# Optimization experiments

Measured on AMD Instinct MI355X. Metric: run time of the kernel, lower is better.

The kernel has to match this reference:

```python
import jax, jax.numpy as jnp
import numpy as np

W_LOAD = 0.01  # config.w_load
CAP_FACTOR = 2  # expert capacity = CAP_FACTOR * tokens * top_k / n_experts


def setup_inputs() -> dict:
    key = jax.random.key(0)
    ks = jax.random.split(key, 8)
    B, T, d, E, dff = 4, 4096, 1024, 8, 4096
    N = B * T
    s = 0.02
    return {
        "x": jax.random.normal(ks[0], (B, T, d), jnp.float32),
        "noise": jax.random.normal(ks[1], (N, E), jnp.float32),
        "gate_w": jax.random.normal(ks[2], (d, E), jnp.float32) * s,
        "noise_w": jax.random.normal(ks[3], (d, E), jnp.float32) * s,
        "w1": jax.random.normal(ks[4], (E, d, dff), jnp.float32) * s,
        "b1": jnp.zeros((E, dff), jnp.float32),
        "w2": jax.random.normal(ks[5], (E, dff, d), jnp.float32) * s,
        "b2": jnp.zeros((E, d), jnp.float32),
        "top_k": 2,
    }


def _moe_forward(x, noise, gate_w, noise_w, w1, b1, w2, b2, top_k):
    B, T, d = x.shape
    N = B * T
    E = gate_w.shape[1]
    xs = x.reshape(N, d)

    # noisy gating
    gate_logits = xs @ gate_w                       # [N, E]
    noise_std = jax.nn.softplus(xs @ noise_w)       # [N, E]
    gate_logits = gate_logits + noise * noise_std

    # load loss: kth-largest logit excluding each expert i
    eye = jnp.eye(E, dtype=bool)
    masked = jnp.where(eye[None, :, :], -jnp.inf, gate_logits[:, None, :])  # [N,E,E]
    kth_excl = jax.lax.top_k(masked, top_k)[0][..., -1]                     # [N,E]
    P = jax.scipy.stats.norm.cdf((gate_logits - kth_excl) / noise_std)
    load = P.sum(axis=0)                            # [E]
    cv = jnp.std(load, ddof=1) / jnp.mean(load)     # torch .std() is unbiased
    load_loss = W_LOAD * cv ** 2

    # top-k routing weights (softmax over selected logits, in fp32)
    topk_vals, sel = jax.lax.top_k(gate_logits, top_k)          # [N,K]
    wts = jax.nn.softmax(topk_vals.astype(jnp.float32), axis=-1).astype(x.dtype)

    # dispatch: flatten (token, slot) pairs, compute position within each expert
    ef = sel.reshape(-1)                            # [N*K] expert id per pair
    tf = jnp.repeat(jnp.arange(N), top_k)           # [N*K] token id per pair
    wf = wts.reshape(-1)                            # [N*K] combine weight
    oh = jax.nn.one_hot(ef, E, dtype=jnp.int32)     # [N*K, E]
    pos = ((jnp.cumsum(oh, axis=0) - oh) * oh).sum(-1)  # slot index within expert

    C = (CAP_FACTOR * N * top_k) // E               # expert capacity (no drops in practice)
    buf = jnp.zeros((E, C, d), x.dtype).at[ef, pos].set(xs[tf], mode="drop")

    # grouped FFN per expert
    h = jax.nn.gelu(jnp.einsum("ecd,edh->ech", buf, w1) + b1[:, None, :], approximate=True)
    y = jnp.einsum("ech,ehd->ecd", h, w2) + b2[:, None, :]

    # combine: gather pair outputs, weight, scatter-add back to tokens
    valid = pos < C
    pair_out = y[ef, jnp.minimum(pos, C - 1)]       # [N*K, d]
    contrib = jnp.where(valid[:, None], wf[:, None] * pair_out, 0.0)
    results = jnp.zeros((N, d), x.dtype).at[tf].add(contrib)
    return results.reshape(B, T, d), load_loss


def reference(x, noise, gate_w, noise_w, w1, b1, w2, b2, top_k):
    return _moe_forward(x, noise, gate_w, noise_w, w1, b1, w2, b2, top_k)
```

## Files before the change

### kernel.cpp

```cpp
#include <hip/hip_runtime.h>
#include <stdint.h>

#define N_TOK   16384
#define DMODEL  1024
#define NEXP    8
#define DFF     4096
#define CAP     8192
#define MAXB    136
#define W_LOAD_C 0.01f

typedef __attribute__((ext_vector_type(8))) short short8;
typedef __attribute__((ext_vector_type(4))) float f32x4;

__device__ __forceinline__ uint16_t f2bf(float f) {
    uint32_t u = __float_as_uint(f);
    uint32_t r = u + 0x7fffu + ((u >> 16) & 1u);
    return (uint16_t)(r >> 16);
}
__device__ __forceinline__ float bf2f(uint16_t u) {
    return __uint_as_float((uint32_t)u << 16);
}

__device__ __forceinline__ float gelu_tanh(float v) {
    float u = 0.7978845608028654f * (v + 0.044715f * v * v * v);
    float ex = __expf(2.0f * u);
    float th = 1.0f - 2.0f / (ex + 1.0f);
    return 0.5f * v * (1.0f + th);
}

__device__ __forceinline__ void glds16(const uint16_t* g, uint16_t* l) {
    __builtin_amdgcn_global_load_lds(
        (const __attribute__((address_space(1))) void*)g,
        (__attribute__((address_space(3))) void*)l, 16, 0, 0);
}

__global__ __launch_bounds__(512) void gating_kernel(
    const float* __restrict__ x, const float* __restrict__ noise,
    const float* __restrict__ gate_w, const float* __restrict__ noise_w,
    int* __restrict__ cnt, float* __restrict__ loadAcc,
    int* __restrict__ rowlist, float* __restrict__ slotw,
    int* __restrict__ tpos0, int* __restrict__ tpos1,
    float* __restrict__ tw0, float* __restrict__ tw1,
    uint16_t* __restrict__ xb)
{
    __shared__ float lp[8][8];
    __shared__ int   se1[8], se2[8];
    __shared__ float sw1[8], sw2[8];

    const int lane = threadIdx.x & 63;
    const int wid  = threadIdx.x >> 6;
    const int t = blockIdx.x * 8 + wid;

    const float* xr = x + (size_t)t * DMODEL;
    uint16_t* xbr = xb + (size_t)t * DMODEL;
    float ag[8] = {0,0,0,0,0,0,0,0};
    float an[8] = {0,0,0,0,0,0,0,0};
    for (int j = 0; j < 16; ++j) {
        int idx = j * 64 + lane;
        float xv = xr[idx];
        xbr[idx] = f2bf(xv);
        const float4* gp  = (const float4*)(gate_w  + idx * 8);
        const float4* np_ = (const float4*)(noise_w + idx * 8);
        float4 g0 = gp[0], g1 = gp[1];
        float4 n0 = np_[0], n1 = np_[1];
        ag[0] += xv * g0.x; ag[1] += xv * g0.y; ag[2] += xv * g0.z; ag[3] += xv * g0.w;
        ag[4] += xv * g1.x; ag[5] += xv * g1.y; ag[6] += xv * g1.z; ag[7] += xv * g1.w;
        an[0] += xv * n0.x; an[1] += xv * n0.y; an[2] += xv * n0.z; an[3] += xv * n0.w;
        an[4] += xv * n1.x; an[5] += xv * n1.y; an[6] += xv * n1.z; an[7] += xv * n1.w;
    }
    #pragma unroll
    for (int m = 32; m >= 1; m >>= 1) {
        #pragma unroll
        for (int e = 0; e < 8; ++e) {
            ag[e] += __shfl_xor(ag[e], m, 64);
            an[e] += __shfl_xor(an[e], m, 64);
        }
    }
    float logit[8], sdv[8];
    #pragma unroll
    for (int e = 0; e < 8; ++e) {
        float a = an[e];
        float sp = (a > 20.0f) ? a : log1pf(expf(a));
        sdv[e] = sp;
        logit[e] = ag[e] + noise[(size_t)t * 8 + e] * sp;
    }
    float v1 = -1e30f, v2 = -1e30f, v3 = -1e30f; int i1 = 0, i2 = 0;
    #pragma unroll
    for (int e = 0; e < 8; ++e) {
        float v = logit[e];
        if (v > v1)      { v3 = v2; v2 = v1; i2 = i1; v1 = v; i1 = e; }
        else if (v > v2) { v3 = v2; v2 = v; i2 = e; }
        else if (v > v3) { v3 = v; }
    }
    if (lane < 8) {
        float kth = (lane == i1 || lane == i2) ? v3 : v2;
        float z = (logit[lane] - kth) / sdv[lane];
        lp[wid][lane] = 0.5f * erfcf(-z * 0.70710678118654752440f);
    }
    if (lane == 0) {
        float e2 = expf(v2 - v1);
        float inv = 1.0f / (1.0f + e2);
        se1[wid] = i1; se2[wid] = i2;
        sw1[wid] = inv; sw2[wid] = e2 * inv;
        tw0[t] = inv; tw1[t] = e2 * inv;
    }
    __syncthreads();
    if (threadIdx.x < 8) {
        int e = threadIdx.x;
        float s = 0.f;
        #pragma unroll
        for (int w = 0; w < 8; ++w) s += lp[w][e];
        atomicAdd(&loadAcc[e], s);
        int m = 0;
        #pragma unroll
        for (int w = 0; w < 8; ++w) m += (se1[w] == e) + (se2[w] == e);
        if (m > 0) {
            int b = atomicAdd(&cnt[e], m);
            #pragma unroll
            for (int w = 0; w < 8; ++w) {
                int tok = blockIdx.x * 8 + w;
                if (se1[w] == e) {
                    if (b < CAP) { rowlist[e * CAP + b] = tok; slotw[e * CAP + b] = sw1[w]; }
                    tpos0[tok] = e * 32768 + b;
                    b++;
                }
                if (se2[w] == e) {
                    if (b < CAP) { rowlist[e * CAP + b] = tok; slotw[e * CAP + b] = sw2[w]; }
                    tpos1[tok] = e * 32768 + b;
                    b++;
                }
            }
        }
    }
}

__global__ void scan_kernel(const int* __restrict__ cnt,
                            int* __restrict__ be, int* __restrict__ brow,
                            int* __restrict__ ebase)
{
    if (threadIdx.x == 0 && blockIdx.x == 0) {
        int idx = 0;
        for (int e = 0; e < NEXP; ++e) {
            int ce = cnt[e]; if (ce > CAP) ce = CAP;
            int nb = (ce + 255) >> 8;
            ebase[e] = idx * 256;
            for (int k = 0; k < nb; ++k) { be[idx] = e; brow[idx] = k * 256; idx++; }
        }
        for (; idx < MAXB; ++idx) { be[idx] = -1; brow[idx] = 0; }
    }
}

__global__ __launch_bounds__(256) void transpose_w_kernel(
    const float* __restrict__ src, uint16_t* __restrict__ dst, int R, int Cc)
{
    __shared__ float tile[32][33];
    const float* s = src + (size_t)blockIdx.z * R * Cc;
    uint16_t*    d = dst + (size_t)blockIdx.z * R * Cc;
    int c0 = blockIdx.x * 32, r0 = blockIdx.y * 32;
    int tx = threadIdx.x & 31, ty = threadIdx.x >> 5;
    #pragma unroll
    for (int rr = ty; rr < 32; rr += 8)
        tile[rr][tx] = s[(size_t)(r0 + rr) * Cc + c0 + tx];
    __syncthreads();
    #pragma unroll
    for (int rr = ty; rr < 32; rr += 8)
        d[(size_t)(c0 + rr) * R + r0 + tx] = f2bf(tile[tx][rr]);
}

template<int KTOT, int GATHER, int GELU, int ATOMIC>
__global__ __launch_bounds__(512, 2) void gemm_kernel(
    const uint16_t* __restrict__ Abase,
    const uint16_t* __restrict__ Bfull,
    const int*      __restrict__ rowlist,
    const float*    __restrict__ slotw,
    const int*      __restrict__ cnt,
    const int*      __restrict__ be,
    const int*      __restrict__ brow,
    const float*    __restrict__ biasFull,
    uint16_t*       __restrict__ OutBf,
    float*          __restrict__ OutF,
    int ncols, int bo)
{
    __shared__ uint16_t lsm[65536];
    __shared__ int   lT[256];
    __shared__ float lW[256];

    const int nwg  = gridDim.x * gridDim.y;
    const int flat = blockIdx.y * gridDim.x + blockIdx.x;
    const int xcd = flat & 7, sid = flat >> 3;
    const int q = nwg >> 3, r8 = nwg & 7;
    const int f2 = (xcd < r8 ? xcd * (q + 1) : r8 * (q + 1) + (xcd - r8) * q) + sid;
    const int nx  = f2 % gridDim.x;
    const int rbi = f2 / gridDim.x;

    const int rb = rbi + bo;
    if (rb >= MAXB) return;
    const int e = be[rb];
    if (e < 0) return;
    const int row0 = brow[rb];
    int ce = cnt[e]; if (ce > CAP) ce = CAP;
    const int n0 = nx * 256;

    const int t = threadIdx.x;
    const int lane = t & 63;
    const int wid  = t >> 6;
    const int fr = lane & 15, ks = lane >> 4;
    const int wr = wid >> 2, wc = wid & 3;

    if (ATOMIC) {
        if (t < 256) {
            int rr = row0 + t;
            int rc = (rr < ce) ? rr : (ce - 1);
            lT[t] = rowlist[e * CAP + rc];
            lW[t] = (rr < ce) ? slotw[e * CAP + rr] : 0.0f;
        }
    }
    __syncthreads();

    const uint16_t* Bp = Bfull + (size_t)e * ncols * KTOT;
    const uint16_t* aSrc[2];
    const uint16_t* bSrc[2];
    int dstA[2], dstB[2];
    #pragma unroll
    for (int i = 0; i < 2; ++i) {
        const int instr = wid + 8 * i;
        const int r = instr * 16 + (lane >> 2);
        const int s = (lane & 3) ^ (r & 3) ^ ((r >> 2) & 3);
        size_t grow;
        if (GATHER) {
            int rr = row0 + r;
            grow = (size_t)rowlist[e * CAP + ((rr < ce) ? rr : (ce - 1))];
        } else {
            grow = (size_t)rbi * 256 + r;
        }
        aSrc[i] = Abase + grow * KTOT + s * 8;
        dstA[i] = instr * 512 + lane * 8;
        bSrc[i] = Bp + (size_t)(n0 + r) * KTOT + s * 8;
        dstB[i] = 8192 + instr * 512 + lane * 8;
    }

    int offA[8], offB[4];
    #pragma unroll
    for (int g = 0; g < 8; ++g) {
        int r = wr * 128 + g * 16 + fr;
        offA[g] = r * 32 + ((ks ^ (r & 3) ^ ((r >> 2) & 3)) * 8);
    }
    #pragma unroll
    for (int n = 0; n < 4; ++n) {
        int c = wc * 64 + n * 16 + fr;
        offB[n] = 8192 + c * 32 + ((ks ^ (c & 3) ^ ((c >> 2) & 3)) * 8);
    }

    f32x4 acc[8][4];
    #pragma unroll
    for (int a = 0; a < 8; ++a)
        #pragma unroll
        for (int b = 0; b < 4; ++b) acc[a][b] = (f32x4){0.f, 0.f, 0.f, 0.f};

    constexpr int NKT = KTOT / 32;

    #pragma unroll
    for (int p = 0; p < 3; ++p) {
        const int ko = p * 32;
        const int bb = p * 16384;
        glds16(aSrc[0] + ko, &lsm[bb + dstA[0]]);
        glds16(aSrc[1] + ko, &lsm[bb + dstA[1]]);
        glds16(bSrc[0] + ko, &lsm[bb + dstB[0]]);
        glds16(bSrc[1] + ko, &lsm[bb + dstB[1]]);
    }
    asm volatile("s_waitcnt vmcnt(8)" ::: "memory");
    __builtin_amdgcn_s_barrier();
    asm volatile("" ::: "memory");

    for (int kt = 0; kt < NKT; ++kt) {
        const int b = kt & 3;
        if (kt + 3 < NKT) {
            const int ko = (kt + 3) * 32;
            const int bb = ((kt + 3) & 3) * 16384;
            glds16(aSrc[0] + ko, &lsm[bb + dstA[0]]);
            glds16(aSrc[1] + ko, &lsm[bb + dstA[1]]);
            glds16(bSrc[0] + ko, &lsm[bb + dstB[0]]);
            glds16(bSrc[1] + ko, &lsm[bb + dstB[1]]);
        }
        const uint16_t* ab = &lsm[b * 16384];
        short8 af[8], bf[4];
        #pragma unroll
        for (int g = 0; g < 8; ++g) af[g] = *(const short8*)(ab + offA[g]);
        #pragma unroll
        for (int n = 0; n < 4; ++n) bf[n] = *(const short8*)(ab + offB[n]);
        __builtin_amdgcn_s_setprio(1);
        #pragma unroll
        for (int mi = 0; mi < 8; ++mi)
            #pragma unroll
            for (int ni = 0; ni < 4; ++ni)
                acc[mi][ni] = __builtin_amdgcn_mfma_f32_16x16x32_bf16(
                    af[mi], bf[ni], acc[mi][ni], 0, 0, 0);
        __builtin_amdgcn_s_setprio(0);
        const int nin = NKT - 1 - kt;
        if (nin >= 3)      asm volatile("s_waitcnt vmcnt(8)" ::: "memory");
        else if (nin == 2) asm volatile("s_waitcnt vmcnt(4)" ::: "memory");
        else if (nin == 1) asm volatile("s_waitcnt vmcnt(0)" ::: "memory");
        __builtin_amdgcn_s_barrier();
        asm volatile("" ::: "memory");
    }

    const float* bias = biasFull + (size_t)e * ncols;
    if (ATOMIC) {
        #pragma unroll
        for (int mi = 0; mi < 8; ++mi) {
            const int rbase = wr * 128 + mi * 16 + ks * 4;
            #pragma unroll
            for (int ni = 0; ni < 4; ++ni) {
                const int c = n0 + wc * 64 + ni * 16 + fr;
                const float bv = bias[c];
                #pragma unroll
                for (int j = 0; j < 4; ++j) {
                    const int rl = rbase + j;
                    if (row0 + rl < ce) {
                        float v = acc[mi][ni][j] + bv;
                        atomicAdd(&OutF[(size_t)lT[rl] * DMODEL + c], lW[rl] * v);
                    }
                }
            }
        }
    } else {
        for (int half = 0; half < 2; ++half) {
            __syncthreads();
            if (wr == half) {
                #pragma unroll
                for (int mi = 0; mi < 8; ++mi) {
                    #pragma unroll
                    for (int ni = 0; ni < 4; ++ni) {
                        const int cl = wc * 64 + ni * 16 + fr;
                        const float bv = bias[n0 + cl];
                        #pragma unroll
                        for (int j = 0; j < 4; ++j) {
                            float v = acc[mi][ni][j] + bv;
                            if (GELU) v = gelu_tanh(v);
                            const int rl2 = mi * 16 + ks * 4 + j;
                            lsm[rl2 * 264 + cl] = f2bf(v);
                        }
                    }
                }
            }
            __syncthreads();
            #pragma unroll
            for (int p = 0; p < 8; ++p) {
                const int r2 = p * 16 + (t >> 5);
                const int cg = (t & 31) * 8;
                short8 v = *(const short8*)&lsm[r2 * 264 + cg];
                *(short8*)&OutBf[((size_t)rbi * 256 + half * 128 + r2) * ncols + n0 + cg] = v;
            }
        }
    }
}

__global__ __launch_bounds__(256) void combine_kernel(
    const uint16_t* __restrict__ y2,
    const int* __restrict__ tpos0, const int* __restrict__ tpos1,
    const float* __restrict__ tw0, const float* __restrict__ tw1,
    const int* __restrict__ ebase, float* __restrict__ out)
{
    const int wid = threadIdx.x >> 6, lane = threadIdx.x & 63;
    const int t = blockIdx.x * 4 + wid;
    const int p0 = tpos0[t], p1 = tpos1[t];
    const int e0 = p0 >> 15, s0 = p0 & 32767;
    const int e1 = p1 >> 15, s1 = p1 & 32767;
    const bool v0 = s0 < CAP, v1 = s1 < CAP;
    const float w0 = v0 ? tw0[t] : 0.0f;
    const float w1 = v1 ? tw1[t] : 0.0f;
    const uint16_t* r0p = y2 + ((size_t)ebase[e0] + (v0 ? s0 : 0)) * DMODEL;
    const uint16_t* r1p = y2 + ((size_t)ebase[e1] + (v1 ? s1 : 0)) * DMODEL;
    float* op = out + (size_t)t * DMODEL;
    #pragma unroll
    for (int half = 0; half < 2; ++half) {
        const int off = half * 512 + lane * 8;
        short8 a = *(const short8*)(r0p + off);
        short8 b = *(const short8*)(r1p + off);
        float4 o0, o1;
        o0.x = w0 * bf2f((uint16_t)a[0]) + w1 * bf2f((uint16_t)b[0]);
        o0.y = w0 * bf2f((uint16_t)a[1]) + w1 * bf2f((uint16_t)b[1]);
        o0.z = w0 * bf2f((uint16_t)a[2]) + w1 * bf2f((uint16_t)b[2]);
        o0.w = w0 * bf2f((uint16_t)a[3]) + w1 * bf2f((uint16_t)b[3]);
        o1.x = w0 * bf2f((uint16_t)a[4]) + w1 * bf2f((uint16_t)b[4]);
        o1.y = w0 * bf2f((uint16_t)a[5]) + w1 * bf2f((uint16_t)b[5]);
        o1.z = w0 * bf2f((uint16_t)a[6]) + w1 * bf2f((uint16_t)b[6]);
        o1.w = w0 * bf2f((uint16_t)a[7]) + w1 * bf2f((uint16_t)b[7]);
        *(float4*)(op + off)     = o0;
        *(float4*)(op + off + 4) = o1;
    }
}

__global__ void finalize_kernel(const float* __restrict__ loadAcc, float* __restrict__ out) {
    if (threadIdx.x == 0) {
        float m = 0.f;
        #pragma unroll
        for (int e = 0; e < 8; ++e) m += loadAcc[e];
        m *= 0.125f;
        float v = 0.f;
        #pragma unroll
        for (int e = 0; e < 8; ++e) { float d0 = loadAcc[e] - m; v += d0 * d0; }
        v *= (1.0f / 7.0f);
        out[(size_t)N_TOK * DMODEL] = W_LOAD_C * v / (m * m);
    }
}

extern "C" void kernel_launch(void* const* d_in, const int* in_sizes, int n_in,
                              void* d_out, int out_size, void* d_ws, size_t ws_size,
                              hipStream_t stream) {
    const float* x       = (const float*)d_in[0];
    const float* noise   = (const float*)d_in[1];
    const float* gate_w  = (const float*)d_in[2];
    const float* noise_w = (const float*)d_in[3];
    const float* w1      = (const float*)d_in[4];
    const float* b1      = (const float*)d_in[5];
    const float* w2      = (const float*)d_in[6];
    const float* b2      = (const float*)d_in[7];
    float* out = (float*)d_out;
    char* ws = (char*)d_ws;

    int*      cnt     = (int*)(ws + 0);
    float*    loadAcc = (float*)(ws + 256);
    int*      ebase   = (int*)(ws + 512);
    int*      be      = (int*)(ws + 1024);
    int*      brow    = (int*)(ws + 2048);
    int*      rowlist = (int*)(ws + 4096);
    int*      tpos0   = (int*)(ws + 266240);
    int*      tpos1   = (int*)(ws + 331776);
    float*    tw0     = (float*)(ws + 397312);
    float*    tw1     = (float*)(ws + 462848);
    float*    slotw   = (float*)(ws + 528384);
    uint16_t* xb      = (uint16_t*)(ws + 790528);
    uint16_t* w1t     = (uint16_t*)(ws + 34344960);
    uint16_t* w2t     = (uint16_t*)(ws + 101453824);
    uint16_t* h       = (uint16_t*)(ws + 168562688);
    const size_t HOFF = 168562688ull;
    const size_t HSZ  = (size_t)MAXB * 256 * DFF * 2;
    uint16_t* y2      = (uint16_t*)(ws + HOFF + HSZ);
    const size_t Y2SZ = (size_t)MAXB * 256 * DMODEL * 2;
    const bool gatherPath = ws_size >= HOFF + HSZ + Y2SZ;

    hipMemsetAsync(ws, 0, 4096, stream);

    gating_kernel<<<2048, 512, 0, stream>>>(x, noise, gate_w, noise_w,
                                            cnt, loadAcc, rowlist, slotw,
                                            tpos0, tpos1, tw0, tw1, xb);
    scan_kernel<<<1, 64, 0, stream>>>(cnt, be, brow, ebase);
    transpose_w_kernel<<<dim3(128, 32, 8), 256, 0, stream>>>(w1, w1t, 1024, 4096);
    transpose_w_kernel<<<dim3(32, 128, 8), 256, 0, stream>>>(w2, w2t, 4096, 1024);
    finalize_kernel<<<1, 64, 0, stream>>>(loadAcc, out);

    if (gatherPath) {
        gemm_kernel<1024, 1, 1, 0><<<dim3(16, MAXB), 512, 0, stream>>>(
            xb, w1t, rowlist, slotw, cnt, be, brow, b1, h, nullptr, DFF, 0);
        gemm_kernel<4096, 0, 0, 0><<<dim3(4, MAXB), 512, 0, stream>>>(
            h, w2t, rowlist, slotw, cnt, be, brow, b2, y2, nullptr, DMODEL, 0);
        combine_kernel<<<4096, 256, 0, stream>>>(y2, tpos0, tpos1, tw0, tw1,
                                                 ebase, out);
    } else {
        hipMemsetAsync(d_out, 0, (size_t)out_size * sizeof(float), stream);
        size_t avail = (ws_size > HOFF) ? ws_size - HOFF : 0;
        int nch = 8, bpc = (MAXB + 7) / 8;
        for (int c = 1; c <= 8; c <<= 1) {
            int b = (MAXB + c - 1) / c;
            if ((size_t)b * 256 * DFF * 2 <= avail) { nch = c; bpc = b; break; }
        }
        for (int c = 0; c < nch; ++c) {
            int bo = c * bpc;
            if (bo >= MAXB) break;
            gemm_kernel<1024, 1, 1, 0><<<dim3(16, bpc), 512, 0, stream>>>(
                xb, w1t, rowlist, slotw, cnt, be, brow, b1, h, nullptr, DFF, bo);
            gemm_kernel<4096, 0, 0, 1><<<dim3(4, bpc), 512, 0, stream>>>(
                h, w2t, rowlist, slotw, cnt, be, brow, b2, nullptr, out, DMODEL, bo);
        }
    }
}
```

Before: 1.069 ms.

## Split GEMM k-step into two phases with interleaved loads and new LDS layout

Restructures the MoE GEMM main loop so each k-tile runs in two halves. Global-to-LDS loads for A and B are issued in separate phases between barriers, and only half the A fragments are held in registers at once, in a ping-pong style schedule. The LDS layout and swizzle change to a new XOR pattern, and launch bounds drop to one workgroup per CU to free registers. This aims to overlap memory traffic with MFMA work and cut LDS bank conflicts, at the cost of extra barriers per iteration and less occupancy.

```diff
diff --git a/kernel.cpp b/kernel.cpp
--- a/kernel.cpp
+++ b/kernel.cpp
@@ -168,7 +168,7 @@
 }
 
 template<int KTOT, int GATHER, int GELU, int ATOMIC>
-__global__ __launch_bounds__(512, 2) void gemm_kernel(
+__global__ __launch_bounds__(512, 1) void gemm_kernel(
     const uint16_t* __restrict__ Abase,
     const uint16_t* __restrict__ Bfull,
     const int*      __restrict__ rowlist,
@@ -201,9 +201,8 @@
     int ce = cnt[e]; if (ce > CAP) ce = CAP;
     const int n0 = nx * 256;
 
-    const int t = threadIdx.x;
-    const int lane = t & 63;
-    const int wid  = t >> 6;
+    const int t    = threadIdx.x;
+    const int lane = t & 63, wid = t >> 6;
     const int fr = lane & 15, ks = lane >> 4;
     const int wr = wid >> 2, wc = wid & 3;
 
@@ -214,42 +213,39 @@
             lT[t] = rowlist[e * CAP + rc];
             lW[t] = (rr < ce) ? slotw[e * CAP + rr] : 0.0f;
         }
-    }
-    __syncthreads();
+        __syncthreads();
+    }
 
     const uint16_t* Bp = Bfull + (size_t)e * ncols * KTOT;
-    const uint16_t* aSrc[2];
-    const uint16_t* bSrc[2];
-    int dstA[2], dstB[2];
-    #pragma unroll
-    for (int i = 0; i < 2; ++i) {
-        const int instr = wid + 8 * i;
-        const int r = instr * 16 + (lane >> 2);
-        const int s = (lane & 3) ^ (r & 3) ^ ((r >> 2) & 3);
-        size_t grow;
-        if (GATHER) {
-            int rr = row0 + r;
-            grow = (size_t)rowlist[e * CAP + ((rr < ce) ? rr : (ce - 1))];
-        } else {
-            grow = (size_t)rbi * 256 + r;
-        }
-        aSrc[i] = Abase + grow * KTOT + s * 8;
-        dstA[i] = instr * 512 + lane * 8;
-        bSrc[i] = Bp + (size_t)(n0 + r) * KTOT + s * 8;
-        dstB[i] = 8192 + instr * 512 + lane * 8;
-    }
-
-    int offA[8], offB[4];
-    #pragma unroll
-    for (int g = 0; g < 8; ++g) {
-        int r = wr * 128 + g * 16 + fr;
-        offA[g] = r * 32 + ((ks ^ (r & 3) ^ ((r >> 2) & 3)) * 8);
-    }
-    #pragma unroll
-    for (int n = 0; n < 4; ++n) {
-        int c = wc * 64 + n * 16 + fr;
-        offB[n] = 8192 + c * 32 + ((ks ^ (c & 3) ^ ((c >> 2) & 3)) * 8);
-    }
+    const int rsub = lane >> 2;
+    const int kof  = ((lane & 3) ^ (((lane >> 5) & 1) << 1)) * 8;
+    const int rowT0 = wid * 16 + rsub;
+    const int rowT1 = 128 + wid * 16 + rsub;
+    size_t gr0, gr1;
+    if (GATHER) {
+        int r0c = row0 + rowT0; r0c = (r0c < ce) ? r0c : (ce - 1);
+        int r1c = row0 + rowT1; r1c = (r1c < ce) ? r1c : (ce - 1);
+        gr0 = (size_t)rowlist[e * CAP + r0c];
+        gr1 = (size_t)rowlist[e * CAP + r1c];
+    } else {
+        gr0 = (size_t)rbi * 256 + rowT0;
+        gr1 = (size_t)rbi * 256 + rowT1;
+    }
+    const uint16_t* srcA0 = Abase + gr0 * KTOT + kof;
+    const uint16_t* srcA1 = Abase + gr1 * KTOT + kof;
+    const uint16_t* srcB0 = Bp + (size_t)(n0 + rowT0) * KTOT + kof;
+    const uint16_t* srcB1 = Bp + (size_t)(n0 + rowT1) * KTOT + kof;
+    const int dA0 = wid * 1024 + lane * 16;
+    const int dA1 = (8 + wid) * 1024 + lane * 16;
+    const int dB0 = 16384 + dA0;
+    const int dB1 = 16384 + dA1;
+
+    const int sw = (ks * 16) ^ ((fr >> 3) << 5);
+    int aOff[8], bOff[4];
+    #pragma unroll
+    for (int m = 0; m < 8; ++m) aOff[m] = (wr * 8 + m) * 1024 + fr * 64 + sw;
+    #pragma unroll
+    for (int n = 0; n < 4; ++n) bOff[n] = 16384 + (wc * 4 + n) * 1024 + fr * 64 + sw;
 
     f32x4 acc[8][4];
     #pragma unroll
@@ -258,48 +254,69 @@
         for (int b = 0; b < 4; ++b) acc[a][b] = (f32x4){0.f, 0.f, 0.f, 0.f};
 
     constexpr int NKT = KTOT / 32;
+    char* lsb = (char*)lsm;
 
     #pragma unroll
     for (int p = 0; p < 3; ++p) {
-        const int ko = p * 32;
-        const int bb = p * 16384;
-        glds16(aSrc[0] + ko, &lsm[bb + dstA[0]]);
-        glds16(aSrc[1] + ko, &lsm[bb + dstA[1]]);
-        glds16(bSrc[0] + ko, &lsm[bb + dstB[0]]);
-        glds16(bSrc[1] + ko, &lsm[bb + dstB[1]]);
+        char* db = lsb + p * 32768;
+        glds16(srcA0 + p * 32, (uint16_t*)(db + dA0));
+        glds16(srcA1 + p * 32, (uint16_t*)(db + dA1));
+        glds16(srcB0 + p * 32, (uint16_t*)(db + dB0));
+        glds16(srcB1 + p * 32, (uint16_t*)(db + dB1));
     }
     asm volatile("s_waitcnt vmcnt(8)" ::: "memory");
     __builtin_amdgcn_s_barrier();
     asm volatile("" ::: "memory");
 
     for (int kt = 0; kt < NKT; ++kt) {
-        const int b = kt & 3;
-        if (kt + 3 < NKT) {
-            const int ko = (kt + 3) * 32;
-            const int bb = ((kt + 3) & 3) * 16384;
-            glds16(aSrc[0] + ko, &lsm[bb + dstA[0]]);
-            glds16(aSrc[1] + ko, &lsm[bb + dstA[1]]);
-            glds16(bSrc[0] + ko, &lsm[bb + dstB[0]]);
-            glds16(bSrc[1] + ko, &lsm[bb + dstB[1]]);
-        }
-        const uint16_t* ab = &lsm[b * 16384];
-        short8 af[8], bf[4];
-        #pragma unroll
-        for (int g = 0; g < 8; ++g) af[g] = *(const short8*)(ab + offA[g]);
-        #pragma unroll
-        for (int n = 0; n < 4; ++n) bf[n] = *(const short8*)(ab + offB[n]);
+        const char* sb = lsb + (kt & 3) * 32768;
+        char* db = lsb + ((kt + 3) & 3) * 32768;
+        const bool st3 = (kt + 3) < NKT;
+        const int ko = (kt + 3) * 32;
+        short8 bf[4], af[4];
+
+        if (st3) {
+            glds16(srcA0 + ko, (uint16_t*)(db + dA0));
+            glds16(srcA1 + ko, (uint16_t*)(db + dA1));
+        }
+        #pragma unroll
+        for (int n = 0; n < 4; ++n) bf[n] = *(const short8*)(sb + bOff[n]);
+        #pragma unroll
+        for (int m = 0; m < 4; ++m) af[m] = *(const short8*)(sb + aOff[m]);
+        asm volatile("" ::: "memory");
+        __builtin_amdgcn_s_barrier();
         __builtin_amdgcn_s_setprio(1);
         #pragma unroll
-        for (int mi = 0; mi < 8; ++mi)
+        for (int m = 0; m < 4; ++m)
             #pragma unroll
-            for (int ni = 0; ni < 4; ++ni)
-                acc[mi][ni] = __builtin_amdgcn_mfma_f32_16x16x32_bf16(
-                    af[mi], bf[ni], acc[mi][ni], 0, 0, 0);
+            for (int n = 0; n < 4; ++n)
+                acc[m][n] = __builtin_amdgcn_mfma_f32_16x16x32_bf16(
+                    af[m], bf[n], acc[m][n], 0, 0, 0);
         __builtin_amdgcn_s_setprio(0);
-        const int nin = NKT - 1 - kt;
-        if (nin >= 3)      asm volatile("s_waitcnt vmcnt(8)" ::: "memory");
-        else if (nin == 2) asm volatile("s_waitcnt vmcnt(4)" ::: "memory");
-        else if (nin == 1) asm volatile("s_waitcnt vmcnt(0)" ::: "memory");
+        asm volatile("" ::: "memory");
+        __builtin_amdgcn_s_barrier();
+
+        if (st3) {
+            glds16(srcB0 + ko, (uint16_t*)(db + dB0));
+            glds16(srcB1 + ko, (uint16_t*)(db + dB1));
+        }
+        #pragma unroll
+        for (int m = 0; m < 4; ++m) af[m] = *(const short8*)(sb + aOff[4 + m]);
+        asm volatile("" ::: "memory");
+        __builtin_amdgcn_s_barrier();
+        __builtin_amdgcn_s_setprio(1);
+        #pragma unroll
+        for (int m = 0; m < 4; ++m)
+            #pragma unroll
+            for (int n = 0; n < 4; ++n)
+                acc[4 + m][n] = __builtin_amdgcn_mfma_f32_16x16x32_bf16(
+                    af[m], bf[n], acc[4 + m][n], 0, 0, 0);
+        __builtin_amdgcn_s_setprio(0);
+        const int rem = NKT - 1 - kt;
+        if (rem >= 3)      asm volatile("s_waitcnt vmcnt(8)" ::: "memory");
+        else if (rem == 2) asm volatile("s_waitcnt vmcnt(4)" ::: "memory");
+        else if (rem == 1) asm volatile("s_waitcnt vmcnt(0)" ::: "memory");
+        asm volatile("" ::: "memory");
         __builtin_amdgcn_s_barrier();
         asm volatile("" ::: "memory");
     }
```

Measured after the change: 1.028 ms. -3.8%, faster.
